# Performance work log

Measured on AMD Instinct MI355X. Metric: run time of the kernel, lower is better.

## Reference

```python
import jax, jax.numpy as jnp
import jax.scipy as jsp
import numpy as np

LAMBDA_1 = 0.1
LAMBDA_2 = 0.005
EPS_DIAG = 1e-6      # jitter added to covariance diagonal
LOG_2PI_CONST = 2 * 3.14159  # torch code uses 3.14159, not math.pi

B, K, D = 262144, 8, 32


def setup_inputs() -> dict:
    key = jax.random.key(0)
    k1, k2, k3 = jax.random.split(key, 3)
    gamma = jax.random.uniform(k1, (B, K), dtype=jnp.float32)
    features = jax.random.normal(k2, (B, D), dtype=jnp.float32)
    reconstruction_error = jax.random.uniform(k3, (B,), dtype=jnp.float32)
    return {"gamma": gamma, "features": features,
            "reconstruction_error": reconstruction_error}


def _gmm_parameters(gamma, features):
    # gamma: [B,K], features: [B,D]
    gsum = jnp.sum(gamma, axis=0)                              # [K]
    phi = jnp.mean(gamma, axis=0)                              # [K]
    mu = jnp.einsum('bk,bd->kd', gamma, features) / (gsum[:, None] + 1e-8)  # [K,D]
    diff = features[:, None, :] - mu[None, :, :]               # [B,K,D]
    sigma = jnp.einsum('bk,bkd,bke->kde', gamma, diff, diff)   # [K,D,D]
    sigma = sigma / (gsum[:, None, None] + 1e-8)
    sigma = sigma + EPS_DIAG * jnp.eye(sigma.shape[-1], dtype=sigma.dtype)[None]
    return phi, mu, sigma, diff


def _energy(diff, phi, sigma):
    # Batched Cholesky over K tiny SPD matrices (sigma is PD by construction).
    feature_dim = sigma.shape[-1]
    L = jnp.linalg.cholesky(sigma)                             # [K,D,D]
    eye = jnp.eye(feature_dim, dtype=sigma.dtype)
    Linv = jax.vmap(lambda l: jsp.linalg.solve_triangular(l, eye, lower=True))(L)
    inv_sigma = jnp.einsum('kij,kil->kjl', Linv, Linv)         # (L L^T)^-1
    log_det = 2.0 * jnp.sum(jnp.log(jnp.diagonal(L, axis1=-2, axis2=-1)), axis=-1)  # [K]
    mahal = jnp.einsum('bkd,kde,bke->bk', diff, inv_sigma, diff)  # [B,K]
    log_2pi = feature_dim * jnp.log(jnp.asarray(LOG_2PI_CONST, dtype=diff.dtype))
    log_prob = -0.5 * (mahal + log_det[None, :] + log_2pi)     # [B,K]
    wlp = jnp.log(phi + 1e-10)[None, :] + log_prob             # [B,K]
    m = jnp.max(wlp, axis=1)                                   # [B]
    sum_exp = jnp.sum(jnp.exp(wlp - m[:, None]), axis=1)
    total_energy = -(m + jnp.log(sum_exp + 1e-10))
    return jnp.where(jnp.isfinite(total_energy), total_energy,
                     jnp.zeros_like(total_energy))


def reference(gamma, features, reconstruction_error):
    phi, mu, sigma, diff = _gmm_parameters(gamma, features)
    reconstruction_loss = jnp.mean(reconstruction_error)
    energy_loss = jnp.mean(_energy(diff, phi, sigma))
    diag = jnp.diagonal(sigma, axis1=-2, axis2=-1)
    singularity_loss = jnp.sum(1.0 / (diag + 1e-8))
    return reconstruction_loss + LAMBDA_1 * energy_loss + LAMBDA_2 * singularity_loss
```

## Files before the change

### kernel.cpp

```cpp
#include <hip/hip_runtime.h>

using v8h  = __attribute__((ext_vector_type(8))) __fp16;
using h2   = __attribute__((ext_vector_type(2))) __fp16;
using v16f = __attribute__((ext_vector_type(16))) float;
using v4f  = __attribute__((ext_vector_type(4))) float;

#define B_SIZE 262144
#define WS_S2    0
#define WS_S1    8192
#define WS_GS    8448
#define WS_SING  8456
#define WS_C1    8464
#define WS_L16   8736
#define WS_ENP   13184
#define WS_RCP   14208
#define WS_PART  15360
#define WS_PART2 2182144
#define PART_STRIDE 8464
#define MOM_BLK  256
#define EN_BLK   1024

union PkU { h2 p[4]; v8h v; };

__device__ __forceinline__ float lane_bcast(float v, int l) {
  return __builtin_bit_cast(float,
      __builtin_amdgcn_readlane(__builtin_bit_cast(int, v), l));
}

__global__ __launch_bounds__(1024, 4) void k_moments(
    const float* __restrict__ gamma, const float* __restrict__ feat,
    float* __restrict__ part) {
  __shared__ float s2l[16 * 1056];
  __shared__ float s1l[16 * 32];
  __shared__ float gsl[16];
  const int tid = threadIdx.x, lane = tid & 63, w = tid >> 6;
  const int k = w & 7, hsel = w >> 3;
  const int c = lane & 31, half = lane >> 5;
  const int base = blockIdx.x * 1024 + hsel * 512;

  v16f acc;
#pragma unroll
  for (int r = 0; r < 16; ++r) acc[r] = 0.f;
  float s1a = 0.f, ga = 0.f;

#pragma unroll 2
  for (int ch = 0; ch < 32; ++ch) {
    const int rb = base + ch * 16 + half * 8;
    float fc[8], g8[8];
#pragma unroll
    for (int j = 0; j < 8; ++j) {
      fc[j] = feat[(size_t)(rb + j) * 32 + c];
      g8[j] = gamma[(size_t)(rb + j) * 8 + k];
    }
    PkU fp, gp;
#pragma unroll
    for (int jj = 0; jj < 4; ++jj) {
      fp.p[jj] = __builtin_amdgcn_cvt_pkrtz(fc[2 * jj], fc[2 * jj + 1]);
      gp.p[jj] = __builtin_amdgcn_cvt_pkrtz(g8[2 * jj], g8[2 * jj + 1]);
    }
#pragma unroll
    for (int j = 0; j < 8; ++j) {
      s1a = fmaf(g8[j], fc[j], s1a);
      ga += g8[j];
    }
    const v8h af = gp.v * fp.v;
    acc = __builtin_amdgcn_mfma_f32_32x32x16_f16(af, fp.v, acc, 0, 0, 0);
  }

#pragma unroll
  for (int r = 0; r < 16; ++r) {
    const int row = (r & 3) + 8 * (r >> 2) + 4 * half;
    s2l[w * 1056 + row * 33 + c] = acc[r];
  }
  s1a += __shfl_xor(s1a, 32);
  ga  += __shfl_xor(ga, 32);
  if (half == 0) s1l[w * 32 + c] = s1a;
  if (lane == 0) gsl[w] = ga;
  __syncthreads();

  float* pb = part + (size_t)blockIdx.x * PART_STRIDE;
  for (int t = tid; t < 8192; t += 1024) {
    const int kk = t >> 10, row = (t >> 5) & 31, cc = t & 31;
    pb[t] = s2l[kk * 1056 + row * 33 + cc] + s2l[(kk + 8) * 1056 + row * 33 + cc];
  }
  if (tid < 256) pb[8192 + tid] = s1l[tid] + s1l[tid + 256];
  if (tid < 8) pb[8448 + tid] = gsl[tid] + gsl[tid + 8];
}

__global__ void k_reduce(const float* __restrict__ part, float* __restrict__ p2) {
  const int t = blockIdx.x * 256 + threadIdx.x;
  if (t >= 8456) return;
  const int y = blockIdx.y;
  float s = 0.f;
#pragma unroll 8
  for (int b = y * 32; b < y * 32 + 32; ++b)
    s += part[(size_t)b * PART_STRIDE + t];
  p2[(size_t)y * PART_STRIDE + t] = s;
}

__global__ void k_reduce2(const float* __restrict__ p2, float* __restrict__ ws) {
  const int t = blockIdx.x * 256 + threadIdx.x;
  if (t >= 8456) return;
  float s = 0.f;
#pragma unroll
  for (int y = 0; y < 8; ++y) s += p2[(size_t)y * PART_STRIDE + t];
  ws[t] = s;
}

__global__ __launch_bounds__(64, 1) void k_prepare(float* __restrict__ ws) {
  __shared__ float T[32 * 33];
  const int k = blockIdx.x;
  const int i = threadIdx.x & 63;
  const int ri = i & 31;
  const bool act = i < 32;

  const float gs = ws[WS_GS + k];
  const float denom = gs + 1e-8f;
  const float rden = __builtin_amdgcn_rcpf(denom);
  const float s1i = ws[WS_S1 + k * 32 + ri];
  const float mu_i = s1i * rden;

  float a[32];
  {
    const float4* s2p = (const float4*)(ws + WS_S2 + k * 1024 + ri * 32);
    float4 q4[8];
#pragma unroll
    for (int t = 0; t < 8; ++t) q4[t] = s2p[t];
#pragma unroll
    for (int t = 0; t < 8; ++t) {
      a[4 * t + 0] = q4[t].x; a[4 * t + 1] = q4[t].y;
      a[4 * t + 2] = q4[t].z; a[4 * t + 3] = q4[t].w;
    }
  }
  float sing = 0.f;
#pragma unroll
  for (int j = 0; j < 32; ++j) {
    const float muj = lane_bcast(mu_i, j);
    const float s1j = lane_bcast(s1i, j);
    float sig = a[j] - mu_i * s1j - muj * s1i + gs * mu_i * muj;
    sig = sig * rden + ((ri == j) ? 1e-6f : 0.f);
    a[j] = sig;
    if (ri == j) sing = __builtin_amdgcn_rcpf(sig + 1e-8f);
  }
  if (!act) sing = 0.f;
#pragma unroll
  for (int m = 1; m < 64; m <<= 1) sing += __shfl_xor(sing, m);
  if (i == 0) ws[WS_SING + k] = sing;

  float logdet = 0.f;
#pragma unroll
  for (int j = 0; j < 32; ++j) {
    const float ajj = lane_bcast(a[j], j);
    const float ljj = __builtin_amdgcn_sqrtf(ajj);
    const float rljj = __builtin_amdgcn_rcpf(ljj);
    logdet += __logf(ajj);
    const float lij = (ri == j) ? ljj : ((ri > j) ? a[j] * rljj : 0.f);
    a[j] = lij;
#pragma unroll
    for (int p = j + 1; p < 32; ++p) {
      const float lpj = lane_bcast(lij, p);
      a[p] = fmaf(-lij, lpj, a[p]);
    }
  }

  const int c = ri;
  float x[32];
#pragma unroll
  for (int r = 0; r < 32; ++r) {
    float s = (r == c) ? 1.f : 0.f;
#pragma unroll
    for (int p = 0; p < r; ++p) {
      const float lrp = lane_bcast(a[p], r);
      s = fmaf(-lrp, x[p], s);
    }
    x[r] = s * __builtin_amdgcn_rcpf(lane_bcast(a[r], r));
  }

  if (act) {
#pragma unroll
    for (int r = 0; r < 32; ++r) T[r * 33 + c] = x[r];
  }
  __syncthreads();
  float xr[32];
#pragma unroll
  for (int p = 0; p < 32; ++p) xr[p] = T[ri * 33 + p];

  __fp16* l16 = (__fp16*)(ws + WS_L16);
  if (act) {
#pragma unroll
    for (int t = 0; t < 4; ++t) {
      PkU h4;
#pragma unroll
      for (int u = 0; u < 4; ++u)
        h4.p[u] = __builtin_amdgcn_cvt_pkrtz(xr[8 * t + 2 * u], xr[8 * t + 2 * u + 1]);
      *(v8h*)(l16 + (size_t)(k * 32 + ri) * 32 + 8 * t) = h4.v;
    }
  }

  float lm = 0.f;
#pragma unroll
  for (int p = 0; p < 32; ++p) lm = fmaf(xr[p], lane_bcast(mu_i, p), lm);

  float lm2 = act ? lm * lm : 0.f;
#pragma unroll
  for (int m = 1; m < 64; m <<= 1) lm2 += __shfl_xor(lm2, m);

  float q = 0.f;
#pragma unroll
  for (int j = 0; j < 32; ++j) q = fmaf(x[j], lane_bcast(lm, j), q);
  if (act) {
    l16[(size_t)(256 + k) * 32 + c] = (__fp16)q;
    l16[(size_t)(264 + k) * 32 + c] = (__fp16)0.f;
  }

  if (i == 0) {
    const float phi = gs * (1.f / (float)B_SIZE);
    ws[WS_C1 + k] =
        __logf(phi + 1e-10f) - 0.5f * (logdet + 32.f * logf(6.28318f)) - 0.5f * lm2;
  }
}

__global__ __launch_bounds__(256, 4) void k_energy(
    const float* __restrict__ feat, const float* __restrict__ rec,
    const float* __restrict__ ws, float* __restrict__ aws) {
  __shared__ float ben[4], brc[4];
  const int tid = threadIdx.x, lane = tid & 63, wv = tid >> 6;
  const int gw = blockIdx.x * 4 + wv;
  const int ROWS = B_SIZE / (EN_BLK * 4);
  const int base = gw * ROWS;
  const int cl = lane & 15, g = lane >> 4;
  const int p0 = g * 8;

  const __fp16* l16 = (const __fp16*)(ws + WS_L16);
  v8h mf[17];
#pragma unroll
  for (int t = 0; t < 17; ++t)
    mf[t] = *(const v8h*)(l16 + (size_t)(16 * t + cl) * 32 + p0);
  float c1[8];
#pragma unroll
  for (int k = 0; k < 8; ++k) c1[k] = ws[WS_C1 + k];

  float en_acc = 0.f, rv_acc = 0.f;
  const v4f zf = {0.f, 0.f, 0.f, 0.f};

  for (int ch = 0; ch < ROWS / 16; ++ch) {
    const int b0 = base + ch * 16;
    const size_t row = (size_t)(b0 + cl) * 32;
    const float4 fa = *(const float4*)(feat + row + p0);
    const float4 fb = *(const float4*)(feat + row + p0 + 4);
    PkU af;
    af.p[0] = __builtin_amdgcn_cvt_pkrtz(fa.x, fa.y);
    af.p[1] = __builtin_amdgcn_cvt_pkrtz(fa.z, fa.w);
    af.p[2] = __builtin_amdgcn_cvt_pkrtz(fb.x, fb.y);
    af.p[3] = __builtin_amdgcn_cvt_pkrtz(fb.z, fb.w);

    float zk[8];
#pragma unroll
    for (int k = 0; k < 8; ++k) zk[k] = 0.f;
    float yq[4];

#pragma unroll
    for (int t = 0; t < 17; ++t) {
      const v4f y = __builtin_amdgcn_mfma_f32_16x16x32_f16(mf[t], af.v, zf, 0, 0, 0);
      if (t < 16) {
#pragma unroll
        for (int r = 0; r < 4; ++r) zk[t >> 1] = fmaf(y[r], y[r], zk[t >> 1]);
      } else {
#pragma unroll
        for (int r = 0; r < 4; ++r) yq[r] = y[r];
      }
    }
#pragma unroll
    for (int m = 16; m < 64; m <<= 1)
#pragma unroll
      for (int k = 0; k < 8; ++k) zk[k] += __shfl_xor(zk[k], m);

    float mx = -3.0e38f, s = 0.f;
#pragma unroll
    for (int k = 0; k < 8; ++k) {
      const float yp = __shfl(yq[k & 3], cl + ((k >> 2) << 4));
      const float w = c1[k] + yp - 0.5f * zk[k];
      const float mn = fmaxf(mx, w);
      s = s * __expf(mx - mn) + __expf(w - mn);
      mx = mn;
    }
    float en = -(mx + __logf(s + 1e-10f));
    en = (en == en && en < 1e38f && en > -1e38f) ? en : 0.f;
    if (lane < 16) {
      en_acc += en;
      rv_acc += rec[b0 + cl];
    }
  }
#pragma unroll
  for (int m = 32; m; m >>= 1) {
    en_acc += __shfl_down(en_acc, m);
    rv_acc += __shfl_down(rv_acc, m);
  }
  if (lane == 0) { ben[wv] = en_acc; brc[wv] = rv_acc; }
  __syncthreads();
  if (tid == 0) {
    aws[WS_ENP + blockIdx.x] = ben[0] + ben[1] + ben[2] + ben[3];
    aws[WS_RCP + blockIdx.x] = brc[0] + brc[1] + brc[2] + brc[3];
  }
}

__global__ void k_final(const float* __restrict__ ws, float* __restrict__ out) {
  __shared__ float r1[256], r2[256];
  const int tid = threadIdx.x;
  float e = 0.f, r = 0.f;
  for (int i = tid; i < EN_BLK; i += 256) {
    e += ws[WS_ENP + i];
    r += ws[WS_RCP + i];
  }
  r1[tid] = e; r2[tid] = r;
  __syncthreads();
  for (int s = 128; s > 0; s >>= 1) {
    if (tid < s) { r1[tid] += r1[tid + s]; r2[tid] += r2[tid + s]; }
    __syncthreads();
  }
  if (tid == 0) {
    float sing = 0.f;
    for (int t = 0; t < 8; ++t) sing += ws[WS_SING + t];
    const float recm = r2[0] * (1.f / (float)B_SIZE);
    const float enm  = r1[0] * (1.f / (float)B_SIZE);
    out[0] = recm + 0.1f * enm + 0.005f * sing;
  }
}

extern "C" void kernel_launch(void* const* d_in, const int* in_sizes, int n_in,
                              void* d_out, int out_size, void* d_ws, size_t ws_size,
                              hipStream_t stream) {
  const float* gamma = (const float*)d_in[0];
  const float* feat  = (const float*)d_in[1];
  const float* rec   = (const float*)d_in[2];
  float* ws = (float*)d_ws;
  float* out = (float*)d_out;

  hipLaunchKernelGGL(k_moments, dim3(MOM_BLK), dim3(1024), 0, stream,
                     gamma, feat, ws + WS_PART);
  hipLaunchKernelGGL(k_reduce, dim3(34, 8), dim3(256), 0, stream,
                     ws + WS_PART, ws + WS_PART2);
  hipLaunchKernelGGL(k_reduce2, dim3(34), dim3(256), 0, stream, ws + WS_PART2, ws);
  hipLaunchKernelGGL(k_prepare, dim3(8), dim3(64), 0, stream, ws);
  hipLaunchKernelGGL(k_energy, dim3(EN_BLK), dim3(256), 0, stream, feat, rec, ws, ws);
  hipLaunchKernelGGL(k_final, dim3(1), dim3(256), 0, stream, ws, out);
}
```

Measured before the change: 132.4 us.

## Stage feature rows through LDS, drop in-block reduction, fold second reduce into prepare

The moments kernel now uses 512-thread blocks with one wave per mixture component. Each wave loads 16 contiguous feature rows with coalesced float4 reads into its own LDS slice, replacing the strided scalar global loads. Partial moments go straight from registers to global memory, so the shared-memory cross-half reduction and its barrier are gone, at the cost of twice as many partial slabs. The reduce2 kernel is removed and k_prepare sums the eight second-level partials itself, saving one launch but making the 8-block prepare kernel do more serial loads.

```diff
diff --git a/kernel.cpp b/kernel.cpp
--- a/kernel.cpp
+++ b/kernel.cpp
@@ -6,7 +6,6 @@
 using v4f  = __attribute__((ext_vector_type(4))) float;
 
 #define B_SIZE 262144
-#define WS_S2    0
 #define WS_S1    8192
 #define WS_GS    8448
 #define WS_SING  8456
@@ -15,9 +14,9 @@
 #define WS_ENP   13184
 #define WS_RCP   14208
 #define WS_PART  15360
-#define WS_PART2 2182144
+#define WS_PART2 4349952
 #define PART_STRIDE 8464
-#define MOM_BLK  256
+#define MOM_BLK  512
 #define EN_BLK   1024
 
 union PkU { h2 p[4]; v8h v; };
@@ -27,31 +26,38 @@
       __builtin_amdgcn_readlane(__builtin_bit_cast(int, v), l));
 }
 
-__global__ __launch_bounds__(1024, 4) void k_moments(
+__global__ __launch_bounds__(512, 4) void k_moments(
     const float* __restrict__ gamma, const float* __restrict__ feat,
     float* __restrict__ part) {
-  __shared__ float s2l[16 * 1056];
-  __shared__ float s1l[16 * 32];
-  __shared__ float gsl[16];
-  const int tid = threadIdx.x, lane = tid & 63, w = tid >> 6;
-  const int k = w & 7, hsel = w >> 3;
+  __shared__ float stg[8][512];
+  const int tid = threadIdx.x, lane = tid & 63, k = tid >> 6;
   const int c = lane & 31, half = lane >> 5;
-  const int base = blockIdx.x * 1024 + hsel * 512;
+  const int base = blockIdx.x * 512;
 
   v16f acc;
 #pragma unroll
   for (int r = 0; r < 16; ++r) acc[r] = 0.f;
   float s1a = 0.f, ga = 0.f;
 
+  float* st = &stg[k][0];
 #pragma unroll 2
   for (int ch = 0; ch < 32; ++ch) {
-    const int rb = base + ch * 16 + half * 8;
-    float fc[8], g8[8];
-#pragma unroll
-    for (int j = 0; j < 8; ++j) {
-      fc[j] = feat[(size_t)(rb + j) * 32 + c];
-      g8[j] = gamma[(size_t)(rb + j) * 8 + k];
-    }
+    const int rb16 = base + ch * 16;
+    const float4* src = (const float4*)(feat + (size_t)rb16 * 32);
+    const float4 va = src[lane];
+    const float4 vb = src[lane + 64];
+    ((float4*)st)[lane] = va;
+    ((float4*)st)[lane + 64] = vb;
+
+    float g8[8];
+#pragma unroll
+    for (int j = 0; j < 8; ++j)
+      g8[j] = gamma[(size_t)(rb16 + half * 8 + j) * 8 + k];
+
+    float fc[8];
+#pragma unroll
+    for (int j = 0; j < 8; ++j) fc[j] = st[(half * 8 + j) * 32 + c];
+
     PkU fp, gp;
 #pragma unroll
     for (int jj = 0; jj < 4; ++jj) {
@@ -67,24 +73,16 @@
     acc = __builtin_amdgcn_mfma_f32_32x32x16_f16(af, fp.v, acc, 0, 0, 0);
   }
 
+  float* pb = part + (size_t)blockIdx.x * PART_STRIDE;
 #pragma unroll
   for (int r = 0; r < 16; ++r) {
     const int row = (r & 3) + 8 * (r >> 2) + 4 * half;
-    s2l[w * 1056 + row * 33 + c] = acc[r];
+    pb[k * 1024 + row * 32 + c] = acc[r];
   }
   s1a += __shfl_xor(s1a, 32);
   ga  += __shfl_xor(ga, 32);
-  if (half == 0) s1l[w * 32 + c] = s1a;
-  if (lane == 0) gsl[w] = ga;
-  __syncthreads();
-
-  float* pb = part + (size_t)blockIdx.x * PART_STRIDE;
-  for (int t = tid; t < 8192; t += 1024) {
-    const int kk = t >> 10, row = (t >> 5) & 31, cc = t & 31;
-    pb[t] = s2l[kk * 1056 + row * 33 + cc] + s2l[(kk + 8) * 1056 + row * 33 + cc];
-  }
-  if (tid < 256) pb[8192 + tid] = s1l[tid] + s1l[tid + 256];
-  if (tid < 8) pb[8448 + tid] = gsl[tid] + gsl[tid + 8];
+  if (half == 0) pb[WS_S1 + k * 32 + c] = s1a;
+  if (lane == 0) pb[WS_GS + k] = ga;
 }
 
 __global__ void k_reduce(const float* __restrict__ part, float* __restrict__ p2) {
@@ -93,45 +91,41 @@
   const int y = blockIdx.y;
   float s = 0.f;
 #pragma unroll 8
-  for (int b = y * 32; b < y * 32 + 32; ++b)
+  for (int b = y * 64; b < y * 64 + 64; ++b)
     s += part[(size_t)b * PART_STRIDE + t];
   p2[(size_t)y * PART_STRIDE + t] = s;
 }
 
-__global__ void k_reduce2(const float* __restrict__ p2, float* __restrict__ ws) {
-  const int t = blockIdx.x * 256 + threadIdx.x;
-  if (t >= 8456) return;
-  float s = 0.f;
-#pragma unroll
-  for (int y = 0; y < 8; ++y) s += p2[(size_t)y * PART_STRIDE + t];
-  ws[t] = s;
-}
-
-__global__ __launch_bounds__(64, 1) void k_prepare(float* __restrict__ ws) {
+__global__ __launch_bounds__(64, 1) void k_prepare(
+    const float* __restrict__ p2, float* __restrict__ ws) {
   __shared__ float T[32 * 33];
   const int k = blockIdx.x;
   const int i = threadIdx.x & 63;
   const int ri = i & 31;
   const bool act = i < 32;
 
-  const float gs = ws[WS_GS + k];
+  float a[32];
+#pragma unroll
+  for (int j = 0; j < 32; ++j) a[j] = 0.f;
+  float s1i = 0.f, gs = 0.f;
+#pragma unroll
+  for (int y = 0; y < 8; ++y) {
+    const float* sl = p2 + (size_t)y * PART_STRIDE;
+    const float4* s2p = (const float4*)(sl + k * 1024 + ri * 32);
+#pragma unroll
+    for (int t = 0; t < 8; ++t) {
+      const float4 q = s2p[t];
+      a[4 * t + 0] += q.x; a[4 * t + 1] += q.y;
+      a[4 * t + 2] += q.z; a[4 * t + 3] += q.w;
+    }
+    s1i += sl[WS_S1 + k * 32 + ri];
+    gs  += sl[WS_GS + k];
+  }
+
   const float denom = gs + 1e-8f;
   const float rden = __builtin_amdgcn_rcpf(denom);
-  const float s1i = ws[WS_S1 + k * 32 + ri];
   const float mu_i = s1i * rden;
 
-  float a[32];
-  {
-    const float4* s2p = (const float4*)(ws + WS_S2 + k * 1024 + ri * 32);
-    float4 q4[8];
-#pragma unroll
-    for (int t = 0; t < 8; ++t) q4[t] = s2p[t];
-#pragma unroll
-    for (int t = 0; t < 8; ++t) {
-      a[4 * t + 0] = q4[t].x; a[4 * t + 1] = q4[t].y;
-      a[4 * t + 2] = q4[t].z; a[4 * t + 3] = q4[t].w;
-    }
-  }
   float sing = 0.f;
 #pragma unroll
   for (int j = 0; j < 32; ++j) {
@@ -336,12 +330,11 @@
   float* ws = (float*)d_ws;
   float* out = (float*)d_out;
 
-  hipLaunchKernelGGL(k_moments, dim3(MOM_BLK), dim3(1024), 0, stream,
+  hipLaunchKernelGGL(k_moments, dim3(MOM_BLK), dim3(512), 0, stream,
                      gamma, feat, ws + WS_PART);
   hipLaunchKernelGGL(k_reduce, dim3(34, 8), dim3(256), 0, stream,
                      ws + WS_PART, ws + WS_PART2);
-  hipLaunchKernelGGL(k_reduce2, dim3(34), dim3(256), 0, stream, ws + WS_PART2, ws);
-  hipLaunchKernelGGL(k_prepare, dim3(8), dim3(64), 0, stream, ws);
+  hipLaunchKernelGGL(k_prepare, dim3(8), dim3(64), 0, stream, ws + WS_PART2, ws);
   hipLaunchKernelGGL(k_energy, dim3(EN_BLK), dim3(256), 0, stream, feat, rec, ws, ws);
   hipLaunchKernelGGL(k_final, dim3(1), dim3(256), 0, stream, ws, out);
 }
```

Result: no change. 133.7 us (+1.0%).
